# Kernel optimization log

Hardware: AMD Instinct MI355X
Metric: run time of the kernel (lower is better)

Reference implementation:

```python
import jax, jax.numpy as jnp
import numpy as np

B, C, H, W = 4, 256, 128, 256
NUM_CODES = 256  # codebook rows; dim_code == C


def setup_inputs() -> dict:
    key = jax.random.key(0)
    k_feat, k_code = jax.random.split(key)
    feature = jax.random.normal(k_feat, (B, C, H, W), dtype=jnp.float32)
    codebook = jax.random.normal(k_code, (NUM_CODES, C), dtype=jnp.float32)
    return {"feature": feature, "codebook": codebook}


def reference(feature, codebook):
    # Faithful to ComminPub.sender core:
    #   weights = (feature_expand * codebooks).sum(dim=2) / (codebooks*codebooks).sum(dim=2)
    # expressed as a contraction over C instead of materializing [B,N,C,H,W].
    code_norm = jnp.sum(codebook * codebook, axis=1)          # [N]
    weights = jnp.einsum('bchw,nc->bnhw', feature, codebook)   # [B,N,H,W]
    weights = weights / code_norm[None, :, None, None]
    # fc_after_rbdc reconstruction: einsum('b n h w, n c -> b c h w', weights, codebook)
    recon = jnp.einsum('bnhw,nc->bchw', weights, codebook)     # [B,C,H,W]
    return recon
```

## Files before the change

kernel.cpp:

```cpp
#include <hip/hip_runtime.h>
#include <hip/hip_bf16.h>
#include <cstdint>

#define CDIM   256
#define NCODES 256
#define HWB    32768
#define BATCH  4
#define BN     64
#define BK     32

typedef __bf16 bf16x8 __attribute__((ext_vector_type(8)));
typedef float  f32x4  __attribute__((ext_vector_type(4)));

__global__ void norms_kernel(const float* __restrict__ cb, float* __restrict__ inv_norm) {
    const int n = blockIdx.x;
    const int lane = threadIdx.x;
    const float* row = cb + n * CDIM;
    float s = 0.f;
#pragma unroll
    for (int c = 0; c < CDIM; c += 64) {
        float v = row[c + lane];
        s += v * v;
    }
#pragma unroll
    for (int off = 32; off > 0; off >>= 1) s += __shfl_down(s, off, 64);
    if (lane == 0) inv_norm[n] = 1.0f / s;
}

__global__ void mmat_kernel(const float* __restrict__ cb, const float* __restrict__ inv_norm,
                            __bf16* __restrict__ Mb) {
    const int i = blockIdx.x;
    const int j = threadIdx.x;
    float acc = 0.f;
#pragma unroll 4
    for (int n = 0; n < NCODES; ++n) {
        acc += (cb[n * CDIM + i] * inv_norm[n]) * cb[n * CDIM + j];
    }
    Mb[i * CDIM + j] = (__bf16)acc;
}

__global__ __launch_bounds__(256, 4) void recon_kernel(
    const float* __restrict__ feat, const __bf16* __restrict__ Mb,
    float* __restrict__ out) {
    __shared__ __align__(16) __bf16 Alds[CDIM * BK];
    __shared__ __align__(16) __bf16 Blds[BN * BK];

    const int tid  = threadIdx.x;
    const int lane = tid & 63;
    const int w    = tid >> 6;
    const int quad = lane >> 4;
    const int l16  = lane & 15;

    const int b  = blockIdx.y;
    const int p0 = blockIdx.x * BN;

    const float* fbase = feat + ((size_t)b * CDIM) * HWB + p0;
    float*       obase = out  + ((size_t)b * CDIM) * HWB + p0;

    f32x4 acc[4][4];
#pragma unroll
    for (int mt = 0; mt < 4; ++mt)
#pragma unroll
        for (int nt = 0; nt < 4; ++nt)
            acc[mt][nt] = (f32x4){0.f, 0.f, 0.f, 0.f};

    const float* fp = fbase + (size_t)(w * 8) * HWB + lane;

    for (int kc = 0; kc < 8; ++kc) {
        float fv[8];
#pragma unroll
        for (int j = 0; j < 8; ++j)
            fv[j] = fp[(size_t)j * HWB];

#pragma unroll
        for (int j = 0; j < 4; ++j) {
            const int gbase = j * 256 + (w << 6);
            const int g = gbase + lane;
            const __bf16* gsrc = Mb + (g >> 2) * CDIM + kc * BK + (g & 3) * 8;
            __builtin_amdgcn_global_load_lds(
                (const __attribute__((address_space(1))) void*)gsrc,
                (__attribute__((address_space(3))) void*)(Alds + (size_t)gbase * 8),
                16, 0, 0);
        }

        bf16x8 pk;
#pragma unroll
        for (int j = 0; j < 8; ++j) pk[j] = (__bf16)fv[j];
        *(bf16x8*)(Blds + lane * BK + w * 8) = pk;

        __syncthreads();

        bf16x8 bfr[4];
#pragma unroll
        for (int nt = 0; nt < 4; ++nt)
            bfr[nt] = *(const bf16x8*)(Blds + (nt * 16 + l16) * BK + quad * 8);
#pragma unroll
        for (int mt = 0; mt < 4; ++mt) {
            bf16x8 af = *(const bf16x8*)(Alds + (w * 64 + mt * 16 + l16) * BK + quad * 8);
#pragma unroll
            for (int nt = 0; nt < 4; ++nt)
                acc[mt][nt] = __builtin_amdgcn_mfma_f32_16x16x32_bf16(
                    af, bfr[nt], acc[mt][nt], 0, 0, 0);
        }
        __syncthreads();
        fp += (size_t)BK * HWB;
    }

#pragma unroll
    for (int mt = 0; mt < 4; ++mt) {
#pragma unroll
        for (int r = 0; r < 4; ++r) {
            const int c = w * 64 + mt * 16 + quad * 4 + r;
            float* orow = obase + (size_t)c * HWB + l16;
#pragma unroll
            for (int nt = 0; nt < 4; ++nt)
                orow[nt * 16] = acc[mt][nt][r];
        }
    }
}

extern "C" void kernel_launch(void* const* d_in, const int* in_sizes, int n_in,
                              void* d_out, int out_size, void* d_ws, size_t ws_size,
                              hipStream_t stream) {
    const float* feat = (const float*)d_in[0];
    const float* cb   = (const float*)d_in[1];
    float* out = (float*)d_out;

    float*  inv_norm = (float*)d_ws;
    __bf16* Mb       = (__bf16*)((char*)d_ws + 1024);

    norms_kernel<<<NCODES, 64, 0, stream>>>(cb, inv_norm);
    mmat_kernel<<<NCODES, CDIM, 0, stream>>>(cb, inv_norm, Mb);

    dim3 grid(HWB / BN, BATCH);
    recon_kernel<<<grid, 256, 0, stream>>>(feat, Mb, out);
}
```

Before: 271.6 us.

## Keep M matrix in registers and double-buffer full-K feature tiles in LDS

The recon kernel is restructured so each wave holds its 32-row slice of the bf16 projection matrix in registers for the whole block. Instead of streaming K chunks of both operands through LDS, it stages an entire 64-pixel by 256-channel feature tile in a double-buffered, XOR-swizzled LDS buffer. Each block loops over four pixel tiles, prefetching the next tile while computing the current one. This removes repeated loads of M from global memory and cuts barriers per tile. The cost is a larger LDS footprint (64KB) and more register pressure, which may lower occupancy.

```diff
diff --git a/kernel.cpp b/kernel.cpp
--- a/kernel.cpp
+++ b/kernel.cpp
@@ -6,11 +6,14 @@
 #define NCODES 256
 #define HWB    32768
 #define BATCH  4
-#define BN     64
-#define BK     32
+#define PX     64
+#define TPB    512
+#define TILES  4
 
 typedef __bf16 bf16x8 __attribute__((ext_vector_type(8)));
 typedef float  f32x4  __attribute__((ext_vector_type(4)));
+
+#define SW(k8, p) ((k8) ^ (((p) & 7) << 3))
 
 __global__ void norms_kernel(const float* __restrict__ cb, float* __restrict__ inv_norm) {
     const int n = blockIdx.x;
@@ -39,83 +42,116 @@
     Mb[i * CDIM + j] = (__bf16)acc;
 }
 
-__global__ __launch_bounds__(256, 4) void recon_kernel(
+__global__ __launch_bounds__(TPB, 4) void recon_kernel(
     const float* __restrict__ feat, const __bf16* __restrict__ Mb,
     float* __restrict__ out) {
-    __shared__ __align__(16) __bf16 Alds[CDIM * BK];
-    __shared__ __align__(16) __bf16 Blds[BN * BK];
+    __shared__ __align__(16) __bf16 Blds[2][PX * CDIM];
 
     const int tid  = threadIdx.x;
     const int lane = tid & 63;
     const int w    = tid >> 6;
     const int quad = lane >> 4;
     const int l16  = lane & 15;
+    const int r0   = w * 32;
 
-    const int b  = blockIdx.y;
-    const int p0 = blockIdx.x * BN;
+    bf16x8 mreg[2][8];
+#pragma unroll
+    for (int mt = 0; mt < 2; ++mt)
+#pragma unroll
+        for (int kc = 0; kc < 8; ++kc)
+            mreg[mt][kc] = *(const bf16x8*)(
+                Mb + (size_t)(r0 + mt * 16 + l16) * CDIM + kc * 32 + quad * 8);
 
-    const float* fbase = feat + ((size_t)b * CDIM) * HWB + p0;
-    float*       obase = out  + ((size_t)b * CDIM) * HWB + p0;
-
-    f32x4 acc[4][4];
+    f32x4 acc[2][4];
 #pragma unroll
-    for (int mt = 0; mt < 4; ++mt)
+    for (int mt = 0; mt < 2; ++mt)
 #pragma unroll
         for (int nt = 0; nt < 4; ++nt)
             acc[mt][nt] = (f32x4){0.f, 0.f, 0.f, 0.f};
 
-    const float* fp = fbase + (size_t)(w * 8) * HWB + lane;
+    const int tile0 = blockIdx.x * TILES;
 
-    for (int kc = 0; kc < 8; ++kc) {
-        float fv[8];
+    {
+        const int t  = tile0;
+        const int b  = t >> 9;
+        const int p0 = (t & 511) << 6;
+        const float* fb = feat + (size_t)b * CDIM * HWB + p0 + lane;
 #pragma unroll
-        for (int j = 0; j < 8; ++j)
-            fv[j] = fp[(size_t)j * HWB];
+        for (int sub = 0; sub < 4; ++sub) {
+            const int k0 = sub * 64 + w * 8;
+            float fv[8];
+#pragma unroll
+            for (int j = 0; j < 8; ++j) fv[j] = fb[(size_t)(k0 + j) * HWB];
+            bf16x8 pk;
+#pragma unroll
+            for (int j = 0; j < 8; ++j) pk[j] = (__bf16)fv[j];
+            *(bf16x8*)(&Blds[0][0] + lane * CDIM + SW(k0, lane)) = pk;
+        }
+    }
+    __syncthreads();
+
+    int cur = 0;
+    for (int ti = 0; ti < TILES; ++ti) {
+        const int t  = tile0 + ti;
+        const int b  = t >> 9;
+        const int p0 = (t & 511) << 6;
+        const bool pf = (ti + 1 < TILES);
+        const int tn = t + 1;
+        const float* fbn = feat + (size_t)(tn >> 9) * CDIM * HWB
+                                + ((tn & 511) << 6) + lane;
+        const __bf16* ldsr = &Blds[cur][0];
+        __bf16*       ldsw = &Blds[cur ^ 1][0];
 
 #pragma unroll
-        for (int j = 0; j < 4; ++j) {
-            const int gbase = j * 256 + (w << 6);
-            const int g = gbase + lane;
-            const __bf16* gsrc = Mb + (g >> 2) * CDIM + kc * BK + (g & 3) * 8;
-            __builtin_amdgcn_global_load_lds(
-                (const __attribute__((address_space(1))) void*)gsrc,
-                (__attribute__((address_space(3))) void*)(Alds + (size_t)gbase * 8),
-                16, 0, 0);
+        for (int sub = 0; sub < 4; ++sub) {
+            const int k0 = sub * 64 + w * 8;
+            float fv[8];
+            if (pf) {
+#pragma unroll
+                for (int j = 0; j < 8; ++j) fv[j] = fbn[(size_t)(k0 + j) * HWB];
+            }
+#pragma unroll
+            for (int kc2 = 0; kc2 < 2; ++kc2) {
+                const int kc = sub * 2 + kc2;
+                bf16x8 bfr[4];
+#pragma unroll
+                for (int nt = 0; nt < 4; ++nt) {
+                    const int row = nt * 16 + l16;
+                    bfr[nt] = *(const bf16x8*)(
+                        ldsr + row * CDIM + SW(kc * 32 + quad * 8, row));
+                }
+#pragma unroll
+                for (int mt = 0; mt < 2; ++mt)
+#pragma unroll
+                    for (int nt = 0; nt < 4; ++nt)
+                        acc[mt][nt] = __builtin_amdgcn_mfma_f32_16x16x32_bf16(
+                            mreg[mt][kc], bfr[nt], acc[mt][nt], 0, 0, 0);
+            }
+            if (pf) {
+                bf16x8 pk;
+#pragma unroll
+                for (int j = 0; j < 8; ++j) pk[j] = (__bf16)fv[j];
+                *(bf16x8*)(ldsw + lane * CDIM + SW(k0, lane)) = pk;
+            }
         }
 
-        bf16x8 pk;
+        float* ob = out + (size_t)b * CDIM * HWB + p0 + l16;
 #pragma unroll
-        for (int j = 0; j < 8; ++j) pk[j] = (__bf16)fv[j];
-        *(bf16x8*)(Blds + lane * BK + w * 8) = pk;
+        for (int mt = 0; mt < 2; ++mt)
+#pragma unroll
+            for (int r = 0; r < 4; ++r) {
+                float* orow = ob + (size_t)(r0 + mt * 16 + quad * 4 + r) * HWB;
+#pragma unroll
+                for (int nt = 0; nt < 4; ++nt) orow[nt * 16] = acc[mt][nt][r];
+            }
+#pragma unroll
+        for (int mt = 0; mt < 2; ++mt)
+#pragma unroll
+            for (int nt = 0; nt < 4; ++nt)
+                acc[mt][nt] = (f32x4){0.f, 0.f, 0.f, 0.f};
 
         __syncthreads();
-
-        bf16x8 bfr[4];
-#pragma unroll
-        for (int nt = 0; nt < 4; ++nt)
-            bfr[nt] = *(const bf16x8*)(Blds + (nt * 16 + l16) * BK + quad * 8);
-#pragma unroll
-        for (int mt = 0; mt < 4; ++mt) {
-            bf16x8 af = *(const bf16x8*)(Alds + (w * 64 + mt * 16 + l16) * BK + quad * 8);
-#pragma unroll
-            for (int nt = 0; nt < 4; ++nt)
-                acc[mt][nt] = __builtin_amdgcn_mfma_f32_16x16x32_bf16(
-                    af, bfr[nt], acc[mt][nt], 0, 0, 0);
-        }
-        __syncthreads();
-        fp += (size_t)BK * HWB;
-    }
-
-#pragma unroll
-    for (int mt = 0; mt < 4; ++mt) {
-#pragma unroll
-        for (int r = 0; r < 4; ++r) {
-            const int c = w * 64 + mt * 16 + quad * 4 + r;
-            float* orow = obase + (size_t)c * HWB + l16;
-#pragma unroll
-            for (int nt = 0; nt < 4; ++nt)
-                orow[nt * 16] = acc[mt][nt][r];
-        }
+        cur ^= 1;
     }
 }
 
@@ -132,6 +168,6 @@
     norms_kernel<<<NCODES, 64, 0, stream>>>(cb, inv_norm);
     mmat_kernel<<<NCODES, CDIM, 0, stream>>>(cb, inv_norm, Mb);
 
-    dim3 grid(HWB / BN, BATCH);
-    recon_kernel<<<grid, 256, 0, stream>>>(feat, Mb, out);
+    const int nblocks = (HWB * BATCH) / (PX * TILES);
+    recon_kernel<<<nblocks, TPB, 0, stream>>>(feat, Mb, out);
 }
```

Result: slower. 362.0 us (+33.3%).

## Double-buffer recon LDS tiles with swizzle and fuse norm into M prep

Applied to the files above, without the earlier changes.

The recon GEMM now double-buffers its A (Mb) and B (feature) LDS tiles, so the global loads for the next K chunk are issued before the current chunk's MFMAs run. Only one barrier per iteration remains. XOR swizzles on the LDS write and read offsets aim to cut bank conflicts. The separate norm and M-matrix kernels are merged into one prep kernel that staggers the scaled codebook column in shared memory, saving a launch. In exchange the recon kernel doubles its LDS use and holds prefetched feature values in registers across the MFMA loop, which may hurt occupancy under launch_bounds(256,4).

```diff
diff --git a/kernel.cpp b/kernel.cpp
--- a/kernel.cpp
+++ b/kernel.cpp
@@ -12,38 +12,34 @@
 typedef __bf16 bf16x8 __attribute__((ext_vector_type(8)));
 typedef float  f32x4  __attribute__((ext_vector_type(4)));
 
-__global__ void norms_kernel(const float* __restrict__ cb, float* __restrict__ inv_norm) {
-    const int n = blockIdx.x;
-    const int lane = threadIdx.x;
-    const float* row = cb + n * CDIM;
-    float s = 0.f;
-#pragma unroll
-    for (int c = 0; c < CDIM; c += 64) {
-        float v = row[c + lane];
-        s += v * v;
-    }
-#pragma unroll
-    for (int off = 32; off > 0; off >>= 1) s += __shfl_down(s, off, 64);
-    if (lane == 0) inv_norm[n] = 1.0f / s;
-}
-
-__global__ void mmat_kernel(const float* __restrict__ cb, const float* __restrict__ inv_norm,
-                            __bf16* __restrict__ Mb) {
+__global__ __launch_bounds__(256) void prep_kernel(const float* __restrict__ cb,
+                                                   __bf16* __restrict__ Mb) {
+    __shared__ float s[NCODES];
     const int i = blockIdx.x;
     const int j = threadIdx.x;
+
+    const float* row = cb + (size_t)j * CDIM;
+    float nrm = 0.f;
+#pragma unroll 8
+    for (int c = 0; c < CDIM; c += 4) {
+        f32x4 v = *(const f32x4*)(row + c);
+        nrm += v[0] * v[0] + v[1] * v[1] + v[2] * v[2] + v[3] * v[3];
+    }
+    s[j] = cb[(size_t)j * CDIM + i] / nrm;
+    __syncthreads();
+
     float acc = 0.f;
-#pragma unroll 4
-    for (int n = 0; n < NCODES; ++n) {
-        acc += (cb[n * CDIM + i] * inv_norm[n]) * cb[n * CDIM + j];
-    }
-    Mb[i * CDIM + j] = (__bf16)acc;
+#pragma unroll 16
+    for (int n = 0; n < NCODES; ++n)
+        acc += s[n] * cb[(size_t)n * CDIM + j];
+    Mb[(size_t)i * CDIM + j] = (__bf16)acc;
 }
 
 __global__ __launch_bounds__(256, 4) void recon_kernel(
     const float* __restrict__ feat, const __bf16* __restrict__ Mb,
     float* __restrict__ out) {
-    __shared__ __align__(16) __bf16 Alds[CDIM * BK];
-    __shared__ __align__(16) __bf16 Blds[BN * BK];
+    __shared__ __align__(16) __bf16 Alds[2][CDIM * BK];
+    __shared__ __align__(16) __bf16 Blds[2][BN * BK];
 
     const int tid  = threadIdx.x;
     const int lane = tid & 63;
@@ -64,46 +60,73 @@
         for (int nt = 0; nt < 4; ++nt)
             acc[mt][nt] = (f32x4){0.f, 0.f, 0.f, 0.f};
 
-    const float* fp = fbase + (size_t)(w * 8) * HWB + lane;
+    const float* fp0 = fbase + (size_t)(w * 8) * HWB + lane;
+    const int bw_off = lane * BK + (w ^ (lane & 3)) * 8;
+    const int qsrcA = (lane & 3) ^ ((lane >> 2) & 3);
+    const int qrd = (quad ^ (l16 & 3)) * 8;
 
-    for (int kc = 0; kc < 8; ++kc) {
+    {
         float fv[8];
 #pragma unroll
-        for (int j = 0; j < 8; ++j)
-            fv[j] = fp[(size_t)j * HWB];
-
+        for (int j = 0; j < 8; ++j) fv[j] = fp0[(size_t)j * HWB];
 #pragma unroll
         for (int j = 0; j < 4; ++j) {
             const int gbase = j * 256 + (w << 6);
-            const int g = gbase + lane;
-            const __bf16* gsrc = Mb + (g >> 2) * CDIM + kc * BK + (g & 3) * 8;
+            const int r = (gbase + lane) >> 2;
+            const __bf16* gsrc = Mb + (size_t)r * CDIM + qsrcA * 8;
             __builtin_amdgcn_global_load_lds(
                 (const __attribute__((address_space(1))) void*)gsrc,
-                (__attribute__((address_space(3))) void*)(Alds + (size_t)gbase * 8),
+                (__attribute__((address_space(3))) void*)(&Alds[0][0] + (size_t)gbase * 8),
                 16, 0, 0);
         }
-
         bf16x8 pk;
 #pragma unroll
         for (int j = 0; j < 8; ++j) pk[j] = (__bf16)fv[j];
-        *(bf16x8*)(Blds + lane * BK + w * 8) = pk;
+        *(bf16x8*)(&Blds[0][0] + bw_off) = pk;
+    }
+    __syncthreads();
 
-        __syncthreads();
+    int cur = 0;
+    for (int kc = 0; kc < 8; ++kc) {
+        const bool pf = (kc + 1 < 8);
+        float fv[8];
+        if (pf) {
+            const float* fp = fp0 + (size_t)(kc + 1) * BK * HWB;
+#pragma unroll
+            for (int j = 0; j < 8; ++j) fv[j] = fp[(size_t)j * HWB];
+#pragma unroll
+            for (int j = 0; j < 4; ++j) {
+                const int gbase = j * 256 + (w << 6);
+                const int r = (gbase + lane) >> 2;
+                const __bf16* gsrc = Mb + (size_t)r * CDIM + (kc + 1) * BK + qsrcA * 8;
+                __builtin_amdgcn_global_load_lds(
+                    (const __attribute__((address_space(1))) void*)gsrc,
+                    (__attribute__((address_space(3))) void*)(&Alds[cur ^ 1][0] + (size_t)gbase * 8),
+                    16, 0, 0);
+            }
+        }
 
         bf16x8 bfr[4];
 #pragma unroll
         for (int nt = 0; nt < 4; ++nt)
-            bfr[nt] = *(const bf16x8*)(Blds + (nt * 16 + l16) * BK + quad * 8);
+            bfr[nt] = *(const bf16x8*)(&Blds[cur][0] + (nt * 16 + l16) * BK + qrd);
 #pragma unroll
         for (int mt = 0; mt < 4; ++mt) {
-            bf16x8 af = *(const bf16x8*)(Alds + (w * 64 + mt * 16 + l16) * BK + quad * 8);
+            bf16x8 af = *(const bf16x8*)(&Alds[cur][0] + (w * 64 + mt * 16 + l16) * BK + qrd);
 #pragma unroll
             for (int nt = 0; nt < 4; ++nt)
                 acc[mt][nt] = __builtin_amdgcn_mfma_f32_16x16x32_bf16(
                     af, bfr[nt], acc[mt][nt], 0, 0, 0);
         }
+
+        if (pf) {
+            bf16x8 pk;
+#pragma unroll
+            for (int j = 0; j < 8; ++j) pk[j] = (__bf16)fv[j];
+            *(bf16x8*)(&Blds[cur ^ 1][0] + bw_off) = pk;
+        }
         __syncthreads();
-        fp += (size_t)BK * HWB;
+        cur ^= 1;
     }
 
 #pragma unroll
@@ -126,11 +149,9 @@
     const float* cb   = (const float*)d_in[1];
     float* out = (float*)d_out;
 
-    float*  inv_norm = (float*)d_ws;
-    __bf16* Mb       = (__bf16*)((char*)d_ws + 1024);
+    __bf16* Mb = (__bf16*)d_ws;
 
-    norms_kernel<<<NCODES, 64, 0, stream>>>(cb, inv_norm);
-    mmat_kernel<<<NCODES, CDIM, 0, stream>>>(cb, inv_norm, Mb);
+    prep_kernel<<<NCODES, 256, 0, stream>>>(cb, Mb);
 
     dim3 grid(HWB / BN, BATCH);
     recon_kernel<<<grid, 256, 0, stream>>>(feat, Mb, out);
```

Result: faster. 253.5 us (-6.7%).
